# Kernel optimization log

Hardware: AMD Instinct MI355X
Metric: run time of the kernel (lower is better)

Reference implementation:

```python
import jax, jax.numpy as jnp
import numpy as np

B, T, C, E, H = 4, 2048, 1024, 8, 4096

def setup_inputs() -> dict:
    key = jax.random.key(0)
    ks = jax.random.split(key, 5)
    x = jax.random.normal(ks[0], (B, T, C), dtype=jnp.float32)
    weights = jax.random.uniform(ks[1], (B, T, 2), dtype=jnp.float32)
    gamma = jnp.ones((C,), dtype=jnp.float32)
    beta = jnp.zeros((C,), dtype=jnp.float32)
    W1 = jax.random.normal(ks[2], (E, C, H), dtype=jnp.float32) * 0.02
    W2 = jax.random.normal(ks[3], (E, H, C), dtype=jnp.float32) * 0.02
    winners = jax.random.randint(ks[4], (B, T, 2), 0, E, dtype=jnp.int32)
    return {"x": x, "weights": weights, "gamma": gamma, "beta": beta,
            "W1": W1, "W2": W2, "winners": winners}

def _layernorm(x, gamma, beta, eps=1e-5):
    mu = jnp.mean(x, axis=-1, keepdims=True)
    var = jnp.var(x, axis=-1, keepdims=True)
    return (x - mu) * jax.lax.rsqrt(var + eps) * gamma + beta

def reference(x, weights, gamma, beta, W1, W2, winners):
    # h = ln2(x); then top-2 MoE dispatch/combine as in CaMoE_Block
    h = _layernorm(x, gamma, beta)          # [B,T,C]
    n_experts = W1.shape[0]
    final_out = jnp.zeros_like(h)
    for e in range(n_experts):
        # per-token combine coefficient: sum over the 2 ranks where winner==e
        coef = jnp.sum(jnp.where(winners == e, weights, 0.0), axis=-1)  # [B,T]
        # RWKV channel-mix FFN: relu(h W1)^2 W2
        hidden = jnp.square(jax.nn.relu(jnp.einsum('btc,ch->bth', h, W1[e])))
        expert_out = jnp.einsum('bth,hc->btc', hidden, W2[e])
        final_out = final_out + coef[..., None] * expert_out
    return x + final_out
```

## Files before the change

### kernel.cpp

```cpp
#include <hip/hip_runtime.h>
#include <stddef.h>

typedef unsigned short u16;
typedef unsigned int u32;

#define B_ 4
#define T_ 2048
#define C_ 1024
#define E_ 8
#define H_ 4096
#define NTOK (B_ * T_)
#define NPAIR (NTOK * 2)
#define BM 128
#define BN 128
#define BK 64
#define KSPLIT 2
#define MAXTILES 136
#define MAXROWS (MAXTILES * 128)

#define NB_C1 2048
#define NB_C2 2048
#define NB_LN NTOK
#define NB_CNT (NPAIR / 256)
#define NB_TID (MAXROWS / 1024)
#define NB_TOTAL (NB_C1 + NB_C2 + NB_LN + NB_CNT + NB_TID)

typedef __bf16 bf16x8 __attribute__((ext_vector_type(8)));
typedef float f32x4 __attribute__((ext_vector_type(4)));
typedef u16 u16x8 __attribute__((ext_vector_type(8)));

__device__ __forceinline__ u16 f2bf(float f) {
    union { float f; u32 u; } c;
    c.f = f;
    u32 r = c.u + 0x7FFFu + ((c.u >> 16) & 1u);
    return (u16)(r >> 16);
}

__device__ __forceinline__ void gld16(const void* g, void* l) {
    __builtin_amdgcn_global_load_lds(
        (const __attribute__((address_space(1))) u32*)g,
        (__attribute__((address_space(3))) u32*)l, 16, 0, 0);
}


__device__ __forceinline__ void ln_body(
    const float* __restrict__ x, const float* __restrict__ gamma,
    const float* __restrict__ beta, float* __restrict__ out,
    u16* __restrict__ h, int token, float* smf) {
    const int t = threadIdx.x;
    const float* xr = x + (size_t)token * C_;
    float4 v = *(const float4*)(xr + t * 4);
    float s = v.x + v.y + v.z + v.w;
    float ss = v.x * v.x + v.y * v.y + v.z * v.z + v.w * v.w;
    #pragma unroll
    for (int off = 32; off > 0; off >>= 1) {
        s += __shfl_down(s, off);
        ss += __shfl_down(ss, off);
    }
    float* ws_s = smf;
    float* ws_q = smf + 4;
    const int wave = t >> 6, lane = t & 63;
    if (lane == 0) { ws_s[wave] = s; ws_q[wave] = ss; }
    __syncthreads();
    float S = ws_s[0] + ws_s[1] + ws_s[2] + ws_s[3];
    float Q = ws_q[0] + ws_q[1] + ws_q[2] + ws_q[3];
    float mu = S * (1.0f / C_);
    float var = Q * (1.0f / C_) - mu * mu;
    float rstd = rsqrtf(var + 1e-5f);
    float4 g = *(const float4*)(gamma + t * 4);
    float4 b = *(const float4*)(beta + t * 4);
    ushort4 hv;
    hv.x = f2bf((v.x - mu) * rstd * g.x + b.x);
    hv.y = f2bf((v.y - mu) * rstd * g.y + b.y);
    hv.z = f2bf((v.z - mu) * rstd * g.z + b.z);
    hv.w = f2bf((v.w - mu) * rstd * g.w + b.w);
    *(float4*)(out + (size_t)token * C_ + t * 4) = v;
    *(ushort4*)(h + (size_t)token * C_ + t * 4) = hv;
}

template <bool PERM>
__device__ __forceinline__ void conv_body(
    const float* __restrict__ in, u16* __restrict__ outp, int K, int N,
    int bid, u16* sm) {
    const int nbx = N >> 8;
    const int nby = K >> 6;
    const int bx = bid % nbx;
    const int by = (bid / nbx) % nby;
    const int e = bid / (nbx * nby);
    const int k0 = by * 64, n0 = bx * 256;
    const int t = threadIdx.x;
    const float* src = in + (size_t)e * K * N;
    u16* dst = outp + (size_t)e * N * K;
    const int cw = t & 63;
    const int rw = t >> 6;
    #pragma unroll
    for (int p = 0; p < 16; ++p) {
        const int r = p * 4 + rw;
        const int kr = PERM ? (((r & 3) << 4) | (r >> 2)) : r;
        float4 v = *(const float4*)(src + (size_t)(k0 + kr) * N + n0 + cw * 4);
        const int base = r * 258 + cw * 4;
        sm[base + 0] = f2bf(v.x);
        sm[base + 1] = f2bf(v.y);
        sm[base + 2] = f2bf(v.z);
        sm[base + 3] = f2bf(v.w);
    }
    __syncthreads();
    const u32* smw = (const u32*)sm;
    const int c = t & 7;
    const int ro = t >> 3;
    #pragma unroll
    for (int p = 0; p < 4; ++p) {
        const int np = p * 32 + ro;
        u16x8 lo, hi;
        #pragma unroll
        for (int m = 0; m < 8; ++m) {
            u32 wv = smw[(c * 8 + m) * 129 + np];
            lo[m] = (u16)(wv & 0xFFFFu);
            hi[m] = (u16)(wv >> 16);
        }
        *(u16x8*)(dst + (size_t)(n0 + 2 * np) * K + k0 + c * 8) = lo;
        *(u16x8*)(dst + (size_t)(n0 + 2 * np + 1) * K + k0 + c * 8) = hi;
    }
}

__device__ __forceinline__ void count_body(
    const int* __restrict__ winners, int* __restrict__ counts, int b, int* lc) {
    if (threadIdx.x < E_) lc[threadIdx.x] = 0;
    __syncthreads();
    atomicAdd(&lc[winners[b * 256 + threadIdx.x]], 1);
    __syncthreads();
    if (threadIdx.x < E_) {
        int c = lc[threadIdx.x];
        if (c) atomicAdd(&counts[threadIdx.x], c);
    }
}

__global__ __launch_bounds__(256) void fused_pre(
    const float* __restrict__ x, const float* __restrict__ gamma,
    const float* __restrict__ beta, float* __restrict__ out,
    u16* __restrict__ h, const int* __restrict__ winners,
    int* __restrict__ counts, const float* __restrict__ W1,
    u16* __restrict__ W1T, const float* __restrict__ W2,
    u16* __restrict__ W2T, int* __restrict__ token_id) {
    __shared__ u16 sm[64 * 258];
    int b = blockIdx.x;
    if (b < NB_C1) { conv_body<false>(W1, W1T, C_, H_, b, sm); return; }
    b -= NB_C1;
    if (b < NB_C2) { conv_body<true>(W2, W2T, H_, C_, b, sm); return; }
    b -= NB_C2;
    if (b < NB_LN) { ln_body(x, gamma, beta, out, h, b, (float*)sm); return; }
    b -= NB_LN;
    if (b < NB_CNT) { count_body(winners, counts, b, (int*)sm); return; }
    b -= NB_CNT;
    const int p = (b * 256 + threadIdx.x) * 4;
    if (p < MAXROWS) *(int4*)(token_id + p) = make_int4(-1, -1, -1, -1);
}

__global__ __launch_bounds__(256) void place_kernel(
    const int* __restrict__ winners, const float* __restrict__ wts,
    const int* __restrict__ counts, int* __restrict__ pos,
    int* __restrict__ token_id, float* __restrict__ pair_w,
    int* __restrict__ tile_expert) {
    __shared__ int po[E_ + 1];
    __shared__ int lcount[E_], lbase[E_];
    const int t = threadIdx.x;
    if (t < E_) lcount[t] = 0;
    if (t == 0) {
        int off = 0;
        po[0] = 0;
        #pragma unroll
        for (int e = 0; e < E_; ++e) {
            off += ((counts[e] + 127) >> 7) << 7;
            po[e + 1] = off;
        }
    }
    __syncthreads();
    if (blockIdx.x == 0 && t < MAXTILES) {
        int r = t * 128;
        int ee = -1;
        if (r < po[E_]) {
            ee = 0;
            while (r >= po[ee + 1]) ++ee;
        }
        tile_expert[t] = ee;
    }
    const int p = blockIdx.x * 256 + t;
    const int e = winners[p];
    const int rank = atomicAdd(&lcount[e], 1);
    __syncthreads();
    if (t < E_) {
        int c = lcount[t];
        lbase[t] = c ? atomicAdd(&pos[t], c) : 0;
    }
    __syncthreads();
    const int slot = po[e] + lbase[e] + rank;
    token_id[slot] = p >> 1;
    pair_w[slot] = wts[p];
}

template <bool PHASE2>
__global__ __launch_bounds__(256, 4) void gemm_kernel(
    const u16* __restrict__ Amat, const u16* __restrict__ Bmat,
    const int* __restrict__ token_id, const float* __restrict__ pair_w,
    const int* __restrict__ tile_expert, u16* __restrict__ hidden,
    float* __restrict__ out, const u16* __restrict__ zeropage) {
    constexpr int Kdim = PHASE2 ? H_ : C_;
    constexpr int KRANGE = PHASE2 ? (H_ / KSPLIT) : C_;
    constexpr int NWGX = PHASE2 ? (C_ / BN) : (H_ / BN);
    constexpr int NWG = NWGX * MAXTILES;

    int bid = blockIdx.y * NWGX + blockIdx.x;
    bid = (bid & 7) * (NWG >> 3) + (bid >> 3);
    const int ct = bid % NWGX;
    const int rt = bid / NWGX;

    const int e = tile_expert[rt];
    if (e < 0) return;
    const int tid = threadIdx.x;
    const int w = tid >> 6;
    const int lane = tid & 63;
    const int n0 = ct * BN;
    const int kbase = PHASE2 ? blockIdx.z * KRANGE : 0;
    const u16* Bb = Bmat + (size_t)e * H_ * C_;

    __shared__ u16 As[BM * BK];
    __shared__ u16 Bs[BN * BK];

    const int sub = lane >> 3;
    const size_t koffB = (size_t)(((lane & 7) ^ sub) * 16);

    const char* abase[4];
    bool aval[4];
    const char* bbase[4];
    u16* adst[4];
    u16* bdst[4];
    #pragma unroll
    for (int j = 0; j < 4; ++j) {
        const int lrow32 = w * 32 + j * 8 + sub;
        const int grow = rt * BM + lrow32;
        if (PHASE2) {
            aval[j] = true;
            abase[j] = (const char*)(Amat + (size_t)grow * Kdim + kbase) + koffB;
        } else {
            int tok = token_id[grow];
            aval[j] = tok >= 0;
            abase[j] = (const char*)(Amat + (size_t)(tok < 0 ? 0 : tok) * Kdim) + koffB;
        }
        bbase[j] = (const char*)(Bb + (size_t)(n0 + lrow32) * Kdim + kbase) + koffB;
        adst[j] = &As[(w * 32 + j * 8) * BK];
        bdst[j] = &Bs[(w * 32 + j * 8) * BK];
    }

    const int wr = w >> 1, wc = w & 1;
    const int lrow = lane & 15;
    const int quad = lane >> 4;
    const int rsw = lrow & 7;

    f32x4 acc[4][4] = {};

    for (int k0 = 0; k0 < KRANGE; k0 += BK) {
        __syncthreads();
        const size_t kb = (size_t)k0 * 2;
        #pragma unroll
        for (int j = 0; j < 4; ++j)
            gld16(aval[j] ? abase[j] + kb : (const char*)zeropage, adst[j]);
        #pragma unroll
        for (int j = 0; j < 4; ++j)
            gld16(bbase[j] + kb, bdst[j]);
        __syncthreads();
        #pragma unroll
        for (int kk = 0; kk < 2; ++kk) {
            bf16x8 af[4], bfv[4];
            #pragma unroll
            for (int mi = 0; mi < 4; ++mi) {
                int row = wr * 64 + mi * 16 + lrow;
                int pch = (kk * 4 + quad) ^ rsw;
                af[mi] = *(const bf16x8*)&As[row * BK + pch * 8];
            }
            #pragma unroll
            for (int ni = 0; ni < 4; ++ni) {
                int row = wc * 64 + ni * 16 + lrow;
                int pch = (kk * 4 + quad) ^ rsw;
                bfv[ni] = *(const bf16x8*)&Bs[row * BK + pch * 8];
            }
            #pragma unroll
            for (int mi = 0; mi < 4; ++mi)
                #pragma unroll
                for (int ni = 0; ni < 4; ++ni)
                    acc[mi][ni] = __builtin_amdgcn_mfma_f32_16x16x32_bf16(
                        af[mi], bfv[ni], acc[mi][ni], 0, 0, 0);
        }
    }

    if (!PHASE2) {
        #pragma unroll
        for (int mi = 0; mi < 4; ++mi) {
            int rbase = rt * BM + wr * 64 + mi * 16 + quad * 4;
            #pragma unroll
            for (int j = 0; j < 4; ++j) {
                ushort4 o;
                float v0 = fmaxf(acc[mi][0][j], 0.0f);
                float v1 = fmaxf(acc[mi][1][j], 0.0f);
                float v2 = fmaxf(acc[mi][2][j], 0.0f);
                float v3 = fmaxf(acc[mi][3][j], 0.0f);
                o.x = f2bf(v0 * v0);
                o.y = f2bf(v1 * v1);
                o.z = f2bf(v2 * v2);
                o.w = f2bf(v3 * v3);
                *(ushort4*)&hidden[(size_t)(rbase + j) * H_ + n0 + wc * 64 + lrow * 4] = o;
            }
        }
    } else {
        #pragma unroll
        for (int mi = 0; mi < 4; ++mi) {
            int rbase = rt * BM + wr * 64 + mi * 16 + quad * 4;
            #pragma unroll
            for (int j = 0; j < 4; ++j) {
                int grow = rbase + j;
                int tok = token_id[grow];
                if (tok < 0) continue;
                float pw = pair_w[grow];
                #pragma unroll
                for (int ni = 0; ni < 4; ++ni) {
                    int col = n0 + wc * 64 + ni * 16 + lrow;
                    atomicAdd(&out[(size_t)tok * C_ + col], pw * acc[mi][ni][j]);
                }
            }
        }
    }
}

extern "C" void kernel_launch(void* const* d_in, const int* in_sizes, int n_in,
                              void* d_out, int out_size, void* d_ws, size_t ws_size,
                              hipStream_t stream) {
    const float* x = (const float*)d_in[0];
    const float* weights = (const float*)d_in[1];
    const float* gamma = (const float*)d_in[2];
    const float* beta = (const float*)d_in[3];
    const float* W1 = (const float*)d_in[4];
    const float* W2 = (const float*)d_in[5];
    const int* winners = (const int*)d_in[6];
    float* out = (float*)d_out;

    char* ws = (char*)d_ws;
    const size_t SZ_H = (size_t)NTOK * C_ * 2;
    const size_t SZ_HID = (size_t)MAXROWS * H_ * 2;
    const size_t SZ_WT = (size_t)E_ * H_ * C_ * 2;
    const size_t OFF_HID = SZ_H;
    const size_t OFF_W1T = OFF_HID + SZ_HID;
    const size_t OFF_W2T = OFF_W1T + SZ_WT;
    const size_t OFF_META = OFF_W2T + SZ_WT;

    u16* h = (u16*)ws;
    u16* hidden = (u16*)(ws + OFF_HID);
    u16* W1T = (u16*)(ws + OFF_W1T);
    u16* W2T = (u16*)(ws + OFF_W2T);
    int* meta = (int*)(ws + OFF_META);
    int* counts = meta;
    int* pos = meta + 8;
    u16* zeropage = (u16*)(meta + 32);
    int* tile_expert = meta + 48;
    int* token_id = meta + 192;
    float* pair_w = (float*)(meta + 192 + MAXROWS);

    hipMemsetAsync(meta, 0, 192 * sizeof(int), stream);

    fused_pre<<<NB_TOTAL, 256, 0, stream>>>(x, gamma, beta, out, h, winners,
                                            counts, W1, W1T, W2, W2T, token_id);
    place_kernel<<<NPAIR / 256, 256, 0, stream>>>(winners, weights, counts, pos,
                                                  token_id, pair_w, tile_expert);
    gemm_kernel<false><<<dim3(H_ / BN, MAXTILES), 256, 0, stream>>>(
        h, W1T, token_id, pair_w, tile_expert, hidden, nullptr, zeropage);
    gemm_kernel<true><<<dim3(C_ / BN, MAXTILES, KSPLIT), 256, 0, stream>>>(
        hidden, W2T, token_id, pair_w, tile_expert, nullptr, out, zeropage);
}
```

Measured before the change: 715.5 us.

## Overlap W2 bf16 conversion with first expert GEMM in one launch

Moves the W2 fp32-to-bf16 transpose/convert blocks out of the pre-processing kernel and appends them to the grid of the first grouped GEMM, so the conversion runs alongside GEMM1 work instead of ahead of it. The GEMM body becomes a device function that takes its block index and shared buffers explicitly. In exchange, GEMM1 blocks now allocate the larger shared buffer sized for the conversion, which can lower occupancy. The conversion blocks also compete with GEMM1 for bandwidth.

```diff
diff --git a/kernel.cpp b/kernel.cpp
--- a/kernel.cpp
+++ b/kernel.cpp
@@ -17,13 +17,14 @@
 #define KSPLIT 2
 #define MAXTILES 136
 #define MAXROWS (MAXTILES * 128)
+#define NWG1 ((H_ / BN) * MAXTILES)
 
 #define NB_C1 2048
 #define NB_C2 2048
 #define NB_LN NTOK
 #define NB_CNT (NPAIR / 256)
 #define NB_TID (MAXROWS / 1024)
-#define NB_TOTAL (NB_C1 + NB_C2 + NB_LN + NB_CNT + NB_TID)
+#define NB_TOTAL (NB_C1 + NB_LN + NB_CNT + NB_TID)
 
 typedef __bf16 bf16x8 __attribute__((ext_vector_type(8)));
 typedef float f32x4 __attribute__((ext_vector_type(4)));
@@ -140,14 +141,11 @@
     const float* __restrict__ beta, float* __restrict__ out,
     u16* __restrict__ h, const int* __restrict__ winners,
     int* __restrict__ counts, const float* __restrict__ W1,
-    u16* __restrict__ W1T, const float* __restrict__ W2,
-    u16* __restrict__ W2T, int* __restrict__ token_id) {
+    u16* __restrict__ W1T, int* __restrict__ token_id) {
     __shared__ u16 sm[64 * 258];
     int b = blockIdx.x;
     if (b < NB_C1) { conv_body<false>(W1, W1T, C_, H_, b, sm); return; }
     b -= NB_C1;
-    if (b < NB_C2) { conv_body<true>(W2, W2T, H_, C_, b, sm); return; }
-    b -= NB_C2;
     if (b < NB_LN) { ln_body(x, gamma, beta, out, h, b, (float*)sm); return; }
     b -= NB_LN;
     if (b < NB_CNT) { count_body(winners, counts, b, (int*)sm); return; }
@@ -199,18 +197,18 @@
 }
 
 template <bool PHASE2>
-__global__ __launch_bounds__(256, 4) void gemm_kernel(
+__device__ __forceinline__ void gemm_body(
     const u16* __restrict__ Amat, const u16* __restrict__ Bmat,
     const int* __restrict__ token_id, const float* __restrict__ pair_w,
     const int* __restrict__ tile_expert, u16* __restrict__ hidden,
-    float* __restrict__ out, const u16* __restrict__ zeropage) {
+    float* __restrict__ out, const u16* __restrict__ zeropage,
+    int bid0, int zi, u16* __restrict__ As, u16* __restrict__ Bs) {
     constexpr int Kdim = PHASE2 ? H_ : C_;
     constexpr int KRANGE = PHASE2 ? (H_ / KSPLIT) : C_;
     constexpr int NWGX = PHASE2 ? (C_ / BN) : (H_ / BN);
     constexpr int NWG = NWGX * MAXTILES;
 
-    int bid = blockIdx.y * NWGX + blockIdx.x;
-    bid = (bid & 7) * (NWG >> 3) + (bid >> 3);
+    int bid = (bid0 & 7) * (NWG >> 3) + (bid0 >> 3);
     const int ct = bid % NWGX;
     const int rt = bid / NWGX;
 
@@ -220,11 +218,8 @@
     const int w = tid >> 6;
     const int lane = tid & 63;
     const int n0 = ct * BN;
-    const int kbase = PHASE2 ? blockIdx.z * KRANGE : 0;
+    const int kbase = PHASE2 ? zi * KRANGE : 0;
     const u16* Bb = Bmat + (size_t)e * H_ * C_;
-
-    __shared__ u16 As[BM * BK];
-    __shared__ u16 Bs[BN * BK];
 
     const int sub = lane >> 3;
     const size_t koffB = (size_t)(((lane & 7) ^ sub) * 16);
@@ -330,6 +325,34 @@
     }
 }
 
+__global__ __launch_bounds__(256, 4) void gemm1_conv(
+    const u16* __restrict__ h, const u16* __restrict__ W1T,
+    const int* __restrict__ token_id, const float* __restrict__ pair_w,
+    const int* __restrict__ tile_expert, u16* __restrict__ hidden,
+    const u16* __restrict__ zeropage, const float* __restrict__ W2,
+    u16* __restrict__ W2T) {
+    __shared__ u16 smu[64 * 258];
+    const int b = blockIdx.x;
+    if (b < NWG1) {
+        gemm_body<false>(h, W1T, token_id, pair_w, tile_expert, hidden,
+                         nullptr, zeropage, b, 0, smu, smu + BM * BK);
+    } else {
+        conv_body<true>(W2, W2T, H_, C_, b - NWG1, smu);
+    }
+}
+
+__global__ __launch_bounds__(256, 4) void gemm2_kernel(
+    const u16* __restrict__ hidden, const u16* __restrict__ W2T,
+    const int* __restrict__ token_id, const float* __restrict__ pair_w,
+    const int* __restrict__ tile_expert, float* __restrict__ out,
+    const u16* __restrict__ zeropage) {
+    __shared__ u16 As[BM * BK];
+    __shared__ u16 Bs[BN * BK];
+    const int bid = blockIdx.y * (C_ / BN) + blockIdx.x;
+    gemm_body<true>(hidden, W2T, token_id, pair_w, tile_expert, nullptr, out,
+                    zeropage, bid, blockIdx.z, As, Bs);
+}
+
 extern "C" void kernel_launch(void* const* d_in, const int* in_sizes, int n_in,
                               void* d_out, int out_size, void* d_ws, size_t ws_size,
                               hipStream_t stream) {
@@ -366,11 +389,11 @@
     hipMemsetAsync(meta, 0, 192 * sizeof(int), stream);
 
     fused_pre<<<NB_TOTAL, 256, 0, stream>>>(x, gamma, beta, out, h, winners,
-                                            counts, W1, W1T, W2, W2T, token_id);
+                                            counts, W1, W1T, token_id);
     place_kernel<<<NPAIR / 256, 256, 0, stream>>>(winners, weights, counts, pos,
                                                   token_id, pair_w, tile_expert);
-    gemm_kernel<false><<<dim3(H_ / BN, MAXTILES), 256, 0, stream>>>(
-        h, W1T, token_id, pair_w, tile_expert, hidden, nullptr, zeropage);
-    gemm_kernel<true><<<dim3(C_ / BN, MAXTILES, KSPLIT), 256, 0, stream>>>(
-        hidden, W2T, token_id, pair_w, tile_expert, nullptr, out, zeropage);
-}
+    gemm1_conv<<<NWG1 + NB_C2, 256, 0, stream>>>(
+        h, W1T, token_id, pair_w, tile_expert, hidden, zeropage, W2, W2T);
+    gemm2_kernel<<<dim3(C_ / BN, MAXTILES, KSPLIT), 256, 0, stream>>>(
+        hidden, W2T, token_id, pair_w, tile_expert, out, zeropage);
+}
```

After: 705.1 us. Within noise of the previous version (-1.5%).
